# Kernel optimization log

Hardware: AMD Instinct MI355X
Metric: run time of the kernel (lower is better)

Reference implementation:

```python
import jax, jax.numpy as jnp
import numpy as np

HEADS = 16
D_MODEL = 1024
D_K = D_MODEL // HEADS
BATCH = 4
SEQ = 1024
NEG_BIG = -1000000000.0


def setup_inputs() -> dict:
    key = jax.random.key(0)
    ks = jax.random.split(key, 7)
    s = 1.0 / np.sqrt(D_MODEL)
    return {
        "q": jax.random.normal(ks[0], (BATCH, SEQ, D_MODEL), jnp.float32),
        "k": jax.random.normal(ks[1], (BATCH, SEQ, D_MODEL), jnp.float32),
        "v": jax.random.normal(ks[2], (BATCH, SEQ, D_MODEL), jnp.float32),
        "Wq": jax.random.normal(ks[3], (D_MODEL, D_MODEL), jnp.float32) * s,
        "Wk": jax.random.normal(ks[4], (D_MODEL, D_MODEL), jnp.float32) * s,
        "Wv": jax.random.normal(ks[5], (D_MODEL, D_MODEL), jnp.float32) * s,
        "Wo": jax.random.normal(ks[6], (D_MODEL, D_MODEL), jnp.float32) * s,
    }


def reference(q, k, v, Wq, Wk, Wv, Wo):
    bs = q.shape[0]
    residual = q
    # torch Linear(bias=False): x @ W.T ; then the module's quirky reshape
    # view(bs, h, -1, d_k) on the contiguous [bs, seq, d_model] buffer.
    qh = (q @ Wq.T).reshape(bs, HEADS, -1, D_K)   # [b, h, s, d_k]
    kh = (k @ Wk.T).reshape(bs, HEADS, -1, D_K)
    vh = (v @ Wv.T).reshape(bs, HEADS, -1, D_K)
    scores = jnp.einsum("bhqd,bhkd->bhqk", qh, kh) / jnp.sqrt(
        jnp.asarray(D_K, qh.dtype))
    # data-dependent mask: exact-zero scores get -1e9 before softmax
    scores = jnp.where(scores == 0, jnp.asarray(NEG_BIG, scores.dtype), scores)
    attn = jax.nn.softmax(scores, axis=-1)  # dropout is identity in eval mode
    out = jnp.einsum("bhqk,bhkd->bhqd", attn, vh)  # [b, h, s, d_k]
    concat = jnp.swapaxes(out, 1, 2).reshape(bs, -1, D_MODEL)
    return concat @ Wo.T + residual
```

## Files before the change

### kernel.cpp

```cpp
#include <hip/hip_runtime.h>
#include <stdint.h>

typedef __bf16 bf16x8 __attribute__((ext_vector_type(8)));
typedef __bf16 bf16x2v __attribute__((ext_vector_type(2)));
typedef float f32x4 __attribute__((ext_vector_type(4)));
typedef uint16_t u16x8 __attribute__((ext_vector_type(8)));
typedef uint16_t u16x4 __attribute__((ext_vector_type(4)));

#define DMODEL 1024
#define K1SC 0.1803368801111244f

__device__ __forceinline__ uint16_t bfc(float f) {
  __bf16 h = (__bf16)f;
  return __builtin_bit_cast(uint16_t, h);
}
__device__ __forceinline__ uint32_t pk32(float a, float b) {
  bf16x2v t = {(__bf16)a, (__bf16)b};
  return __builtin_bit_cast(uint32_t, t);
}
__device__ __forceinline__ void gld16(const void* src, void* dst) {
  __builtin_amdgcn_global_load_lds((const __attribute__((address_space(1))) void*)src,
                                   (__attribute__((address_space(3))) void*)dst, 16, 0, 0);
}

__global__ void cvt_all_kernel(const float* __restrict__ q, const float* __restrict__ k,
                               const float* __restrict__ v, const float* __restrict__ Wq,
                               const float* __restrict__ Wk, const float* __restrict__ Wv,
                               const float* __restrict__ Wo, uint16_t* __restrict__ qb,
                               uint16_t* __restrict__ kb, uint16_t* __restrict__ vb,
                               uint16_t* __restrict__ Wqb, uint16_t* __restrict__ Wkb,
                               uint16_t* __restrict__ Wvb, uint16_t* __restrict__ Wob) {
  int bid = blockIdx.x;
  const float* src;
  uint16_t* dst;
  int off;
  if (bid < 12288) {
    int s = bid >> 12;
    src = s == 0 ? q : (s == 1 ? k : v);
    dst = s == 0 ? qb : (s == 1 ? kb : vb);
    off = bid & 4095;
  } else {
    int r = bid - 12288;
    int s = r >> 10;
    src = s == 0 ? Wq : (s == 1 ? Wk : (s == 2 ? Wv : Wo));
    dst = s == 0 ? Wqb : (s == 1 ? Wkb : (s == 2 ? Wvb : Wob));
    off = r & 1023;
  }
  int i = off * 256 + threadIdx.x;
  f32x4 x = ((const f32x4*)src)[i];
  u16x4 r;
#pragma unroll
  for (int j = 0; j < 4; ++j) r[j] = bfc(x[j]);
  ((u16x4*)dst)[i] = r;
}

__global__ __launch_bounds__(256, 2)
void gemm_qkv_kernel(const uint16_t* __restrict__ A0, const uint16_t* __restrict__ A1,
                     const uint16_t* __restrict__ A2, const uint16_t* __restrict__ W0,
                     const uint16_t* __restrict__ W1, const uint16_t* __restrict__ W2,
                     uint16_t* __restrict__ C0, uint16_t* __restrict__ C1,
                     uint16_t* __restrict__ C2) {
  const int z = blockIdx.z;
  const uint16_t* A = z == 0 ? A0 : (z == 1 ? A1 : A2);
  const uint16_t* Bw = z == 0 ? W0 : (z == 1 ? W1 : W2);
  uint16_t* C = z == 0 ? C0 : (z == 1 ? C1 : C2);
  const float osc = (z == 0) ? K1SC : 1.0f;
  __shared__ __align__(16) uint16_t As[2][128 * 32];
  __shared__ __align__(16) uint16_t Bs[2][128 * 32];
  const int t = threadIdx.x;
  const int lane = t & 63;
  const int w = t >> 6;
  const int wr = w >> 1, wc = w & 1;
  const int m0 = blockIdx.y * 128, n0 = blockIdx.x * 128;
  const int lr = lane & 15, ksl = lane >> 4;

  f32x4 acc[4][4];
#pragma unroll
  for (int m = 0; m < 4; ++m)
#pragma unroll
    for (int n = 0; n < 4; ++n) acc[m][n] = (f32x4){0.f, 0.f, 0.f, 0.f};

  auto stage = [&](int buf, int k0) {
#pragma unroll
    for (int cc = 0; cc < 2; ++cc) {
      int idx = cc * 256 + t;
      int row = idx >> 2, sl = idx & 3;
      gld16(A + (size_t)(m0 + row) * DMODEL + k0 + sl * 8, &As[buf][idx * 8]);
      gld16(Bw + (size_t)(n0 + row) * DMODEL + k0 + sl * 8, &Bs[buf][idx * 8]);
    }
  };

  stage(0, 0);
  __syncthreads();

  int cur = 0;
#pragma unroll 1
  for (int kt = 0; kt < 32; ++kt) {
    if (kt < 31) stage(cur ^ 1, (kt + 1) * 32);
    bf16x8 af[4], bfv[4];
#pragma unroll
    for (int m = 0; m < 4; ++m)
      af[m] = *(const bf16x8*)&As[cur][(wr * 64 + m * 16 + lr) * 32 + ksl * 8];
#pragma unroll
    for (int n = 0; n < 4; ++n)
      bfv[n] = *(const bf16x8*)&Bs[cur][(wc * 64 + n * 16 + lr) * 32 + ksl * 8];
    __builtin_amdgcn_s_setprio(1);
#pragma unroll
    for (int m = 0; m < 4; ++m)
#pragma unroll
      for (int n = 0; n < 4; ++n)
        acc[m][n] = __builtin_amdgcn_mfma_f32_16x16x32_bf16(af[m], bfv[n], acc[m][n], 0, 0, 0);
    __builtin_amdgcn_s_setprio(0);
    __syncthreads();
    cur ^= 1;
  }

#pragma unroll
  for (int m = 0; m < 4; ++m) {
#pragma unroll
    for (int n = 0; n < 4; ++n) {
      int col = n0 + wc * 64 + n * 16 + lr;
#pragma unroll
      for (int r = 0; r < 4; ++r) {
        int row = m0 + wr * 64 + m * 16 + ksl * 4 + r;
        C[(size_t)row * DMODEL + col] = bfc(acc[m][n][r] * osc);
      }
    }
  }
}

__global__ __launch_bounds__(256, 2)
void gemm_bt_kernel(const uint16_t* __restrict__ A, const uint16_t* __restrict__ Bw,
                    float* __restrict__ Cf, const float* __restrict__ resid) {
  __shared__ __align__(16) uint16_t As[2][64 * 32];
  __shared__ __align__(16) uint16_t Bs[2][128 * 32];
  const int t = threadIdx.x;
  const int lane = t & 63;
  const int w = t >> 6;
  const int wr = w >> 1, wc = w & 1;
  const int m0 = blockIdx.y * 64, n0 = blockIdx.x * 128;
  const int lr = lane & 15, ksl = lane >> 4;

  f32x4 acc[2][4];
#pragma unroll
  for (int m = 0; m < 2; ++m)
#pragma unroll
    for (int n = 0; n < 4; ++n) acc[m][n] = (f32x4){0.f, 0.f, 0.f, 0.f};

  {
    int row = t >> 2, sl = t & 3;
    gld16(A + (size_t)(m0 + row) * DMODEL + sl * 8, &As[0][t * 8]);
#pragma unroll
    for (int cc = 0; cc < 2; ++cc) {
      int c = t + cc * 256;
      int rb = c >> 2, slb = c & 3;
      gld16(Bw + (size_t)(n0 + rb) * DMODEL + slb * 8, &Bs[0][c * 8]);
    }
  }
  __syncthreads();

  int cur = 0;
#pragma unroll 1
  for (int kt = 0; kt < 32; ++kt) {
    if (kt < 31) {
      int k0 = (kt + 1) * 32;
      int nb = cur ^ 1;
      int row = t >> 2, sl = t & 3;
      gld16(A + (size_t)(m0 + row) * DMODEL + k0 + sl * 8, &As[nb][t * 8]);
#pragma unroll
      for (int cc = 0; cc < 2; ++cc) {
        int c = t + cc * 256;
        int rb = c >> 2, slb = c & 3;
        gld16(Bw + (size_t)(n0 + rb) * DMODEL + k0 + slb * 8, &Bs[nb][c * 8]);
      }
    }
    bf16x8 af[2], bfv[4];
#pragma unroll
    for (int m = 0; m < 2; ++m)
      af[m] = *(const bf16x8*)&As[cur][(wr * 32 + m * 16 + lr) * 32 + ksl * 8];
#pragma unroll
    for (int n = 0; n < 4; ++n)
      bfv[n] = *(const bf16x8*)&Bs[cur][(wc * 64 + n * 16 + lr) * 32 + ksl * 8];
    __builtin_amdgcn_s_setprio(1);
#pragma unroll
    for (int m = 0; m < 2; ++m)
#pragma unroll
      for (int n = 0; n < 4; ++n)
        acc[m][n] = __builtin_amdgcn_mfma_f32_16x16x32_bf16(af[m], bfv[n], acc[m][n], 0, 0, 0);
    __builtin_amdgcn_s_setprio(0);
    __syncthreads();
    cur ^= 1;
  }

#pragma unroll
  for (int m = 0; m < 2; ++m) {
#pragma unroll
    for (int n = 0; n < 4; ++n) {
      int col = n0 + wc * 64 + n * 16 + lr;
#pragma unroll
      for (int r = 0; r < 4; ++r) {
        int row = m0 + wr * 32 + m * 16 + ksl * 4 + r;
        size_t idx = (size_t)row * DMODEL + col;
        Cf[idx] = acc[m][n][r] + resid[idx];
      }
    }
  }
}

__global__ __launch_bounds__(256, 2)
void attn_mfma_kernel(const uint16_t* __restrict__ Pq, const uint16_t* __restrict__ Pk,
                      const uint16_t* __restrict__ Pv, uint16_t* __restrict__ Cc) {
  __shared__ __align__(16) uint16_t Ks[2][64 * 64];
  __shared__ __align__(16) uint16_t Vts[2][64 * 64];
  __shared__ __align__(16) uint16_t Ps[4][16 * 64];

  const int t = threadIdx.x;
  const int w = t >> 6;
  const int lane = t & 63;
  const int lr = lane & 15;
  const int ksl = lane >> 4;
  const int qt = blockIdx.x;
  const int bh = blockIdx.y;
  const int b = bh >> 4, h = bh & 15;

  const uint16_t* Qb = Pq + (size_t)bh * 65536 + (size_t)qt * 64 * 64;
  const uint16_t* Kb = Pk + (size_t)bh * 65536;
  const uint16_t* Vb = Pv + (size_t)bh * 65536;

  bf16x8 qf[2];
  {
    const uint16_t* qrow = Qb + (size_t)(w * 16 + lr) * 64 + ksl * 8;
    qf[0] = *(const bf16x8*)(qrow);
    qf[1] = *(const bf16x8*)(qrow + 32);
  }

  f32x4 Oa[4];
#pragma unroll
  for (int n = 0; n < 4; ++n) Oa[n] = (f32x4){0.f, 0.f, 0.f, 0.f};
  f32x4 lsum4 = {0.f, 0.f, 0.f, 0.f};

  const int p2 = t & 31;
  const int c8 = t >> 5;
  const int sw = (lr & 7) << 4;
  u16x8 va, vb2;

  auto stageK = [&](int buf, int kt) {
#pragma unroll
    for (int cc = 0; cc < 2; ++cc) {
      int idx = cc * 256 + t;
      int row = idx >> 3;
      int bo = (idx & 7) * 16;
      int srcb = bo ^ ((row & 7) << 4);
      gld16(Kb + (size_t)(kt * 64 + row) * 64 + (srcb >> 1), &Ks[buf][idx * 8]);
    }
  };
  auto loadV = [&](int kt) {
    const uint16_t* s0 = Vb + (size_t)(kt * 64 + p2 * 2) * 64 + c8 * 8;
    va = *(const u16x8*)s0;
    vb2 = *(const u16x8*)(s0 + 64);
  };
  auto writeV = [&](int buf) {
    char* base = (char*)&Vts[buf][0];
#pragma unroll
    for (int i = 0; i < 8; ++i) {
      int d = c8 * 8 + i;
      uint32_t val = (uint32_t)va[i] | ((uint32_t)vb2[i] << 16);
      *(uint32_t*)(base + d * 128 + ((p2 * 4) ^ ((d & 7) << 4))) = val;
    }
  };

  stageK(0, 0);
  loadV(0);
  writeV(0);
  __syncthreads();

  int cur = 0;
#pragma unroll 1
  for (int kt = 0; kt < 16; ++kt) {
    if (kt < 15) { stageK(cur ^ 1, kt + 1); loadV(kt + 1); }

    f32x4 S[4];
#pragma unroll
    for (int n = 0; n < 4; ++n) S[n] = (f32x4){0.f, 0.f, 0.f, 0.f};
    __builtin_amdgcn_s_setprio(1);
#pragma unroll
    for (int n = 0; n < 4; ++n) {
      const char* kbp = (const char*)&Ks[cur][0] + (n * 16 + lr) * 128;
#pragma unroll
      for (int c = 0; c < 2; ++c) {
        bf16x8 kf = *(const bf16x8*)(kbp + ((c * 64 + ksl * 16) ^ sw));
        S[n] = __builtin_amdgcn_mfma_f32_16x16x32_bf16(kf, qf[c], S[n], 0, 0, 0);
      }
    }
    __builtin_amdgcn_s_setprio(0);

    f32x4 psum = {0.f, 0.f, 0.f, 0.f};
    f32x4 p4[4];
#pragma unroll
    for (int n = 0; n < 4; ++n) {
#pragma unroll
      for (int r = 0; r < 4; ++r) {
        float x = S[n][r];
        float e = __builtin_amdgcn_exp2f(x);
        p4[n][r] = (x == 0.f) ? 0.f : e;
      }
      psum += p4[n];
    }
    lsum4 += psum;

    char* pb = (char*)&Ps[w][0] + lr * 128;
#pragma unroll
    for (int n = 0; n < 4; ++n) {
      int co = (n * 16 + ksl * 4) * 2;
      *(uint32_t*)(pb + (co ^ sw)) = pk32(p4[n][0], p4[n][1]);
      *(uint32_t*)(pb + ((co + 4) ^ sw)) = pk32(p4[n][2], p4[n][3]);
    }

    __builtin_amdgcn_s_setprio(1);
#pragma unroll
    for (int c = 0; c < 2; ++c) {
      bf16x8 pf = *(const bf16x8*)(pb + ((c * 64 + ksl * 16) ^ sw));
#pragma unroll
      for (int n = 0; n < 4; ++n) {
        const char* vbp = (const char*)&Vts[cur][0] + (n * 16 + lr) * 128;
        bf16x8 vf = *(const bf16x8*)(vbp + ((c * 64 + ksl * 16) ^ sw));
        Oa[n] = __builtin_amdgcn_mfma_f32_16x16x32_bf16(pf, vf, Oa[n], 0, 0, 0);
      }
    }
    __builtin_amdgcn_s_setprio(0);

    if (kt < 15) writeV(cur ^ 1);
    __syncthreads();
    cur ^= 1;
  }

  float lrow = (lsum4[0] + lsum4[1]) + (lsum4[2] + lsum4[3]);
  lrow += __shfl_xor(lrow, 16);
  lrow += __shfl_xor(lrow, 32);
  f32x4 inv4;
#pragma unroll
  for (int r = 0; r < 4; ++r) inv4[r] = 1.f / __shfl(lrow, ksl * 4 + r);

  uint16_t* dst = Cc + (size_t)b * 1048576 + (size_t)(qt * 64 + w * 16) * 1024 + h * 64;
#pragma unroll
  for (int r = 0; r < 4; ++r) {
    int qq = ksl * 4 + r;
#pragma unroll
    for (int n = 0; n < 4; ++n) {
      dst[qq * 1024 + n * 16 + lr] = bfc(Oa[n][r] * inv4[r]);
    }
  }
}

extern "C" void kernel_launch(void* const* d_in, const int* in_sizes, int n_in,
                              void* d_out, int out_size, void* d_ws, size_t ws_size,
                              hipStream_t stream) {
  const float* q  = (const float*)d_in[0];
  const float* k  = (const float*)d_in[1];
  const float* v  = (const float*)d_in[2];
  const float* Wq = (const float*)d_in[3];
  const float* Wk = (const float*)d_in[4];
  const float* Wv = (const float*)d_in[5];
  const float* Wo = (const float*)d_in[6];
  float* out = (float*)d_out;
  char* ws = (char*)d_ws;
  const size_t MB = 1u << 20;
  uint16_t* qb  = (uint16_t*)(ws + 0 * MB);
  uint16_t* kb  = (uint16_t*)(ws + 8 * MB);
  uint16_t* vb  = (uint16_t*)(ws + 16 * MB);
  uint16_t* Wqb = (uint16_t*)(ws + 24 * MB);
  uint16_t* Wkb = (uint16_t*)(ws + 26 * MB);
  uint16_t* Wvb = (uint16_t*)(ws + 28 * MB);
  uint16_t* Wob = (uint16_t*)(ws + 30 * MB);
  uint16_t* Pq  = (uint16_t*)(ws + 32 * MB);
  uint16_t* Pk  = (uint16_t*)(ws + 40 * MB);
  uint16_t* Pv  = (uint16_t*)(ws + 48 * MB);
  uint16_t* Cc  = (uint16_t*)(ws + 56 * MB);

  cvt_all_kernel<<<16384, 256, 0, stream>>>(q, k, v, Wq, Wk, Wv, Wo,
                                            qb, kb, vb, Wqb, Wkb, Wvb, Wob);

  gemm_qkv_kernel<<<dim3(8, 32, 3), 256, 0, stream>>>(qb, kb, vb, Wqb, Wkb, Wvb,
                                                      Pq, Pk, Pv);

  attn_mfma_kernel<<<dim3(16, 64), 256, 0, stream>>>(Pq, Pk, Pv, Cc);

  gemm_bt_kernel<<<dim3(8, 64), 256, 0, stream>>>(Cc, Wob, out, q);
}
```

Measured before the change: 116.9 us.

## Deepen GEMM K-tiles to 64 with XOR-swizzled LDS and XCD-aware block remapping

Both projection GEMMs now stage 64-wide K tiles, which halves the number of main-loop iterations and barriers. Each 16-byte chunk's K offset is XOR-swizzled by row so the LDS fragment reads avoid bank conflicts. Blocks are launched on a 1D grid and remapped so that consecutive tiles land on the same XCD, for better L2 reuse. The output GEMM also grows from 64x128 to 128x128 tiles, which doubles LDS use per block and halves the grid to 256 blocks, risking lower occupancy and fewer waves in flight.

```diff
diff --git a/kernel.cpp b/kernel.cpp
--- a/kernel.cpp
+++ b/kernel.cpp
@@ -60,19 +60,25 @@
                      const uint16_t* __restrict__ W1, const uint16_t* __restrict__ W2,
                      uint16_t* __restrict__ C0, uint16_t* __restrict__ C1,
                      uint16_t* __restrict__ C2) {
-  const int z = blockIdx.z;
+  int orig = blockIdx.x;
+  int lin = (orig & 7) * 96 + (orig >> 3);
+  int z = lin >> 8;
+  int rem = lin & 255;
+  int m0 = (rem >> 3) * 128, n0 = (rem & 7) * 128;
+
   const uint16_t* A = z == 0 ? A0 : (z == 1 ? A1 : A2);
   const uint16_t* Bw = z == 0 ? W0 : (z == 1 ? W1 : W2);
   uint16_t* C = z == 0 ? C0 : (z == 1 ? C1 : C2);
   const float osc = (z == 0) ? K1SC : 1.0f;
-  __shared__ __align__(16) uint16_t As[2][128 * 32];
-  __shared__ __align__(16) uint16_t Bs[2][128 * 32];
+
+  __shared__ __align__(16) uint16_t As[2][128 * 64];
+  __shared__ __align__(16) uint16_t Bs[2][128 * 64];
   const int t = threadIdx.x;
   const int lane = t & 63;
   const int w = t >> 6;
   const int wr = w >> 1, wc = w & 1;
-  const int m0 = blockIdx.y * 128, n0 = blockIdx.x * 128;
   const int lr = lane & 15, ksl = lane >> 4;
+  const int sw = (lr & 7) << 4;
 
   f32x4 acc[4][4];
 #pragma unroll
@@ -82,11 +88,18 @@
 
   auto stage = [&](int buf, int k0) {
 #pragma unroll
-    for (int cc = 0; cc < 2; ++cc) {
+    for (int cc = 0; cc < 4; ++cc) {
       int idx = cc * 256 + t;
-      int row = idx >> 2, sl = idx & 3;
-      gld16(A + (size_t)(m0 + row) * DMODEL + k0 + sl * 8, &As[buf][idx * 8]);
-      gld16(Bw + (size_t)(n0 + row) * DMODEL + k0 + sl * 8, &Bs[buf][idx * 8]);
+      int row = idx >> 3, ch = idx & 7;
+      int so = ((ch * 16) ^ ((row & 7) << 4)) >> 1;
+      gld16(A + (size_t)(m0 + row) * DMODEL + k0 + so, &As[buf][idx * 8]);
+    }
+#pragma unroll
+    for (int cc = 0; cc < 4; ++cc) {
+      int idx = cc * 256 + t;
+      int row = idx >> 3, ch = idx & 7;
+      int so = ((ch * 16) ^ ((row & 7) << 4)) >> 1;
+      gld16(Bw + (size_t)(n0 + row) * DMODEL + k0 + so, &Bs[buf][idx * 8]);
     }
   };
 
@@ -95,21 +108,29 @@
 
   int cur = 0;
 #pragma unroll 1
-  for (int kt = 0; kt < 32; ++kt) {
-    if (kt < 31) stage(cur ^ 1, (kt + 1) * 32);
-    bf16x8 af[4], bfv[4];
-#pragma unroll
-    for (int m = 0; m < 4; ++m)
-      af[m] = *(const bf16x8*)&As[cur][(wr * 64 + m * 16 + lr) * 32 + ksl * 8];
-#pragma unroll
-    for (int n = 0; n < 4; ++n)
-      bfv[n] = *(const bf16x8*)&Bs[cur][(wc * 64 + n * 16 + lr) * 32 + ksl * 8];
+  for (int kt = 0; kt < 16; ++kt) {
+    if (kt < 15) stage(cur ^ 1, (kt + 1) * 64);
+    const char* Ab = (const char*)&As[cur][0];
+    const char* Bb = (const char*)&Bs[cur][0];
+    bf16x8 af[2][4], bfv[2][4];
+#pragma unroll
+    for (int c = 0; c < 2; ++c) {
+      int co = ((c * 4 + ksl) * 16) ^ sw;
+#pragma unroll
+      for (int m = 0; m < 4; ++m)
+        af[c][m] = *(const bf16x8*)(Ab + (wr * 64 + m * 16 + lr) * 128 + co);
+#pragma unroll
+      for (int n = 0; n < 4; ++n)
+        bfv[c][n] = *(const bf16x8*)(Bb + (wc * 64 + n * 16 + lr) * 128 + co);
+    }
     __builtin_amdgcn_s_setprio(1);
 #pragma unroll
-    for (int m = 0; m < 4; ++m)
-#pragma unroll
-      for (int n = 0; n < 4; ++n)
-        acc[m][n] = __builtin_amdgcn_mfma_f32_16x16x32_bf16(af[m], bfv[n], acc[m][n], 0, 0, 0);
+    for (int c = 0; c < 2; ++c)
+#pragma unroll
+      for (int m = 0; m < 4; ++m)
+#pragma unroll
+        for (int n = 0; n < 4; ++n)
+          acc[m][n] = __builtin_amdgcn_mfma_f32_16x16x32_bf16(af[c][m], bfv[c][n], acc[m][n], 0, 0, 0);
     __builtin_amdgcn_s_setprio(0);
     __syncthreads();
     cur ^= 1;
@@ -130,76 +151,85 @@
 }
 
 __global__ __launch_bounds__(256, 2)
-void gemm_bt_kernel(const uint16_t* __restrict__ A, const uint16_t* __restrict__ Bw,
-                    float* __restrict__ Cf, const float* __restrict__ resid) {
-  __shared__ __align__(16) uint16_t As[2][64 * 32];
-  __shared__ __align__(16) uint16_t Bs[2][128 * 32];
+void gemm_o_kernel(const uint16_t* __restrict__ A, const uint16_t* __restrict__ Bw,
+                   float* __restrict__ Cf, const float* __restrict__ resid) {
+  int orig = blockIdx.x;
+  int lin = (orig & 7) * 32 + (orig >> 3);
+  int m0 = (lin >> 3) * 128, n0 = (lin & 7) * 128;
+
+  __shared__ __align__(16) uint16_t As[2][128 * 64];
+  __shared__ __align__(16) uint16_t Bs[2][128 * 64];
   const int t = threadIdx.x;
   const int lane = t & 63;
   const int w = t >> 6;
   const int wr = w >> 1, wc = w & 1;
-  const int m0 = blockIdx.y * 64, n0 = blockIdx.x * 128;
   const int lr = lane & 15, ksl = lane >> 4;
-
-  f32x4 acc[2][4];
-#pragma unroll
-  for (int m = 0; m < 2; ++m)
+  const int sw = (lr & 7) << 4;
+
+  f32x4 acc[4][4];
+#pragma unroll
+  for (int m = 0; m < 4; ++m)
 #pragma unroll
     for (int n = 0; n < 4; ++n) acc[m][n] = (f32x4){0.f, 0.f, 0.f, 0.f};
 
-  {
-    int row = t >> 2, sl = t & 3;
-    gld16(A + (size_t)(m0 + row) * DMODEL + sl * 8, &As[0][t * 8]);
-#pragma unroll
-    for (int cc = 0; cc < 2; ++cc) {
-      int c = t + cc * 256;
-      int rb = c >> 2, slb = c & 3;
-      gld16(Bw + (size_t)(n0 + rb) * DMODEL + slb * 8, &Bs[0][c * 8]);
-    }
-  }
+  auto stage = [&](int buf, int k0) {
+#pragma unroll
+    for (int cc = 0; cc < 4; ++cc) {
+      int idx = cc * 256 + t;
+      int row = idx >> 3, ch = idx & 7;
+      int so = ((ch * 16) ^ ((row & 7) << 4)) >> 1;
+      gld16(A + (size_t)(m0 + row) * DMODEL + k0 + so, &As[buf][idx * 8]);
+    }
+#pragma unroll
+    for (int cc = 0; cc < 4; ++cc) {
+      int idx = cc * 256 + t;
+      int row = idx >> 3, ch = idx & 7;
+      int so = ((ch * 16) ^ ((row & 7) << 4)) >> 1;
+      gld16(Bw + (size_t)(n0 + row) * DMODEL + k0 + so, &Bs[buf][idx * 8]);
+    }
+  };
+
+  stage(0, 0);
   __syncthreads();
 
   int cur = 0;
 #pragma unroll 1
-  for (int kt = 0; kt < 32; ++kt) {
-    if (kt < 31) {
-      int k0 = (kt + 1) * 32;
-      int nb = cur ^ 1;
-      int row = t >> 2, sl = t & 3;
-      gld16(A + (size_t)(m0 + row) * DMODEL + k0 + sl * 8, &As[nb][t * 8]);
-#pragma unroll
-      for (int cc = 0; cc < 2; ++cc) {
-        int c = t + cc * 256;
-        int rb = c >> 2, slb = c & 3;
-        gld16(Bw + (size_t)(n0 + rb) * DMODEL + k0 + slb * 8, &Bs[nb][c * 8]);
-      }
-    }
-    bf16x8 af[2], bfv[4];
-#pragma unroll
-    for (int m = 0; m < 2; ++m)
-      af[m] = *(const bf16x8*)&As[cur][(wr * 32 + m * 16 + lr) * 32 + ksl * 8];
-#pragma unroll
-    for (int n = 0; n < 4; ++n)
-      bfv[n] = *(const bf16x8*)&Bs[cur][(wc * 64 + n * 16 + lr) * 32 + ksl * 8];
+  for (int kt = 0; kt < 16; ++kt) {
+    if (kt < 15) stage(cur ^ 1, (kt + 1) * 64);
+    const char* Ab = (const char*)&As[cur][0];
+    const char* Bb = (const char*)&Bs[cur][0];
+    bf16x8 af[2][4], bfv[2][4];
+#pragma unroll
+    for (int c = 0; c < 2; ++c) {
+      int co = ((c * 4 + ksl) * 16) ^ sw;
+#pragma unroll
+      for (int m = 0; m < 4; ++m)
+        af[c][m] = *(const bf16x8*)(Ab + (wr * 64 + m * 16 + lr) * 128 + co);
+#pragma unroll
+      for (int n = 0; n < 4; ++n)
+        bfv[c][n] = *(const bf16x8*)(Bb + (wc * 64 + n * 16 + lr) * 128 + co);
+    }
     __builtin_amdgcn_s_setprio(1);
 #pragma unroll
-    for (int m = 0; m < 2; ++m)
-#pragma unroll
-      for (int n = 0; n < 4; ++n)
-        acc[m][n] = __builtin_amdgcn_mfma_f32_16x16x32_bf16(af[m], bfv[n], acc[m][n], 0, 0, 0);
+    for (int c = 0; c < 2; ++c)
+#pragma unroll
+      for (int m = 0; m < 4; ++m)
+#pragma unroll
+        for (int n = 0; n < 4; ++n)
+          acc[m][n] = __builtin_amdgcn_mfma_f32_16x16x32_bf16(af[c][m], bfv[c][n], acc[m][n], 0, 0, 0);
     __builtin_amdgcn_s_setprio(0);
     __syncthreads();
     cur ^= 1;
   }
 
 #pragma unroll
-  for (int m = 0; m < 2; ++m) {
+  for (int m = 0; m < 4; ++m) {
 #pragma unroll
     for (int n = 0; n < 4; ++n) {
       int col = n0 + wc * 64 + n * 16 + lr;
 #pragma unroll
       for (int r = 0; r < 4; ++r) {
-        int row = m0 + wr * 32 + m * 16 + ksl * 4 + r;
+        int row = m0 + wr * 64 + m * 16 + ksl * 4 + r;
         size_t idx = (size_t)row * DMODEL + col;
         Cf[idx] = acc[m][n][r] + resid[idx];
       }
@@ -380,10 +410,10 @@
   cvt_all_kernel<<<16384, 256, 0, stream>>>(q, k, v, Wq, Wk, Wv, Wo,
                                             qb, kb, vb, Wqb, Wkb, Wvb, Wob);
 
-  gemm_qkv_kernel<<<dim3(8, 32, 3), 256, 0, stream>>>(qb, kb, vb, Wqb, Wkb, Wvb,
-                                                      Pq, Pk, Pv);
+  gemm_qkv_kernel<<<768, 256, 0, stream>>>(qb, kb, vb, Wqb, Wkb, Wvb,
+                                           Pq, Pk, Pv);
 
   attn_mfma_kernel<<<dim3(16, 64), 256, 0, stream>>>(Pq, Pk, Pv, Cc);
 
-  gemm_bt_kernel<<<dim3(8, 64), 256, 0, stream>>>(Cc, Wob, out, q);
-}
+  gemm_o_kernel<<<256, 256, 0, stream>>>(Cc, Wob, out, q);
+}
```

Result: faster. 112.8 us (-3.5%).

## Swizzle GEMM LDS layout and remap block IDs for XCD locality

Applied to the files above, without the earlier changes.

Applies an XOR swizzle to the 16-byte chunks staged into LDS by both GEMM kernels, so the per-lane fragment reads avoid bank conflicts. All three main kernels now launch on a 1D grid and remap block IDs so consecutive logical tiles land on the same XCD (stride-8 round robin), which is meant to improve L2 reuse of shared A/B rows and K/V tiles. Swizzle correctness depends on the load-side and read-side XOR patterns matching, and the remap assumes an 8-XCD dispatch order.

```diff
diff --git a/kernel.cpp b/kernel.cpp
--- a/kernel.cpp
+++ b/kernel.cpp
@@ -60,19 +60,25 @@
                      const uint16_t* __restrict__ W1, const uint16_t* __restrict__ W2,
                      uint16_t* __restrict__ C0, uint16_t* __restrict__ C1,
                      uint16_t* __restrict__ C2) {
-  const int z = blockIdx.z;
+  int orig = blockIdx.x;
+  int lin = (orig & 7) * 96 + (orig >> 3);
+  int z = lin >> 8;
+  int rem = lin & 255;
+  int m0 = (rem >> 3) * 128, n0 = (rem & 7) * 128;
+
   const uint16_t* A = z == 0 ? A0 : (z == 1 ? A1 : A2);
   const uint16_t* Bw = z == 0 ? W0 : (z == 1 ? W1 : W2);
   uint16_t* C = z == 0 ? C0 : (z == 1 ? C1 : C2);
   const float osc = (z == 0) ? K1SC : 1.0f;
+
   __shared__ __align__(16) uint16_t As[2][128 * 32];
   __shared__ __align__(16) uint16_t Bs[2][128 * 32];
   const int t = threadIdx.x;
   const int lane = t & 63;
   const int w = t >> 6;
   const int wr = w >> 1, wc = w & 1;
-  const int m0 = blockIdx.y * 128, n0 = blockIdx.x * 128;
   const int lr = lane & 15, ksl = lane >> 4;
+  const int sw2 = (lr & 3) << 4;
 
   f32x4 acc[4][4];
 #pragma unroll
@@ -84,9 +90,16 @@
 #pragma unroll
     for (int cc = 0; cc < 2; ++cc) {
       int idx = cc * 256 + t;
-      int row = idx >> 2, sl = idx & 3;
-      gld16(A + (size_t)(m0 + row) * DMODEL + k0 + sl * 8, &As[buf][idx * 8]);
-      gld16(Bw + (size_t)(n0 + row) * DMODEL + k0 + sl * 8, &Bs[buf][idx * 8]);
+      int row = idx >> 2, ch = idx & 3;
+      int so = ((ch * 16) ^ ((row & 3) << 4)) >> 1;
+      gld16(A + (size_t)(m0 + row) * DMODEL + k0 + so, &As[buf][idx * 8]);
+    }
+#pragma unroll
+    for (int cc = 0; cc < 2; ++cc) {
+      int idx = cc * 256 + t;
+      int row = idx >> 2, ch = idx & 3;
+      int so = ((ch * 16) ^ ((row & 3) << 4)) >> 1;
+      gld16(Bw + (size_t)(n0 + row) * DMODEL + k0 + so, &Bs[buf][idx * 8]);
     }
   };
 
@@ -97,13 +110,16 @@
 #pragma unroll 1
   for (int kt = 0; kt < 32; ++kt) {
     if (kt < 31) stage(cur ^ 1, (kt + 1) * 32);
+    const char* Ab = (const char*)&As[cur][0];
+    const char* Bb = (const char*)&Bs[cur][0];
+    const int co = (ksl * 16) ^ sw2;
     bf16x8 af[4], bfv[4];
 #pragma unroll
     for (int m = 0; m < 4; ++m)
-      af[m] = *(const bf16x8*)&As[cur][(wr * 64 + m * 16 + lr) * 32 + ksl * 8];
+      af[m] = *(const bf16x8*)(Ab + (wr * 64 + m * 16 + lr) * 64 + co);
 #pragma unroll
     for (int n = 0; n < 4; ++n)
-      bfv[n] = *(const bf16x8*)&Bs[cur][(wc * 64 + n * 16 + lr) * 32 + ksl * 8];
+      bfv[n] = *(const bf16x8*)(Bb + (wc * 64 + n * 16 + lr) * 64 + co);
     __builtin_amdgcn_s_setprio(1);
 #pragma unroll
     for (int m = 0; m < 4; ++m)
@@ -130,16 +146,20 @@
 }
 
 __global__ __launch_bounds__(256, 2)
-void gemm_bt_kernel(const uint16_t* __restrict__ A, const uint16_t* __restrict__ Bw,
-                    float* __restrict__ Cf, const float* __restrict__ resid) {
+void gemm_o_kernel(const uint16_t* __restrict__ A, const uint16_t* __restrict__ Bw,
+                   float* __restrict__ Cf, const float* __restrict__ resid) {
+  int orig = blockIdx.x;
+  int lin = (orig & 7) * 64 + (orig >> 3);
+  int m0 = (lin >> 3) * 64, n0 = (lin & 7) * 128;
+
   __shared__ __align__(16) uint16_t As[2][64 * 32];
   __shared__ __align__(16) uint16_t Bs[2][128 * 32];
   const int t = threadIdx.x;
   const int lane = t & 63;
   const int w = t >> 6;
   const int wr = w >> 1, wc = w & 1;
-  const int m0 = blockIdx.y * 64, n0 = blockIdx.x * 128;
   const int lr = lane & 15, ksl = lane >> 4;
+  const int sw2 = (lr & 3) << 4;
 
   f32x4 acc[2][4];
 #pragma unroll
@@ -147,40 +167,38 @@
 #pragma unroll
     for (int n = 0; n < 4; ++n) acc[m][n] = (f32x4){0.f, 0.f, 0.f, 0.f};
 
-  {
-    int row = t >> 2, sl = t & 3;
-    gld16(A + (size_t)(m0 + row) * DMODEL + sl * 8, &As[0][t * 8]);
+  auto stage = [&](int buf, int k0) {
+    {
+      int row = t >> 2, ch = t & 3;
+      int so = ((ch * 16) ^ ((row & 3) << 4)) >> 1;
+      gld16(A + (size_t)(m0 + row) * DMODEL + k0 + so, &As[buf][t * 8]);
+    }
 #pragma unroll
     for (int cc = 0; cc < 2; ++cc) {
-      int c = t + cc * 256;
-      int rb = c >> 2, slb = c & 3;
-      gld16(Bw + (size_t)(n0 + rb) * DMODEL + slb * 8, &Bs[0][c * 8]);
-    }
-  }
+      int idx = cc * 256 + t;
+      int row = idx >> 2, ch = idx & 3;
+      int so = ((ch * 16) ^ ((row & 3) << 4)) >> 1;
+      gld16(Bw + (size_t)(n0 + row) * DMODEL + k0 + so, &Bs[buf][idx * 8]);
+    }
+  };
+
+  stage(0, 0);
   __syncthreads();
 
   int cur = 0;
 #pragma unroll 1
   for (int kt = 0; kt < 32; ++kt) {
-    if (kt < 31) {
-      int k0 = (kt + 1) * 32;
-      int nb = cur ^ 1;
-      int row = t >> 2, sl = t & 3;
-      gld16(A + (size_t)(m0 + row) * DMODEL + k0 + sl * 8, &As[nb][t * 8]);
-#pragma unroll
-      for (int cc = 0; cc < 2; ++cc) {
-        int c = t + cc * 256;
-        int rb = c >> 2, slb = c & 3;
-        gld16(Bw + (size_t)(n0 + rb) * DMODEL + k0 + slb * 8, &Bs[nb][c * 8]);
-      }
-    }
+    if (kt < 31) stage(cur ^ 1, (kt + 1) * 32);
+    const char* Ab = (const char*)&As[cur][0];
+    const char* Bb = (const char*)&Bs[cur][0];
+    const int co = (ksl * 16) ^ sw2;
     bf16x8 af[2], bfv[4];
 #pragma unroll
     for (int m = 0; m < 2; ++m)
-      af[m] = *(const bf16x8*)&As[cur][(wr * 32 + m * 16 + lr) * 32 + ksl * 8];
+      af[m] = *(const bf16x8*)(Ab + (wr * 32 + m * 16 + lr) * 64 + co);
 #pragma unroll
     for (int n = 0; n < 4; ++n)
-      bfv[n] = *(const bf16x8*)&Bs[cur][(wc * 64 + n * 16 + lr) * 32 + ksl * 8];
+      bfv[n] = *(const bf16x8*)(Bb + (wc * 64 + n * 16 + lr) * 64 + co);
     __builtin_amdgcn_s_setprio(1);
 #pragma unroll
     for (int m = 0; m < 2; ++m)
@@ -219,8 +237,9 @@
   const int lane = t & 63;
   const int lr = lane & 15;
   const int ksl = lane >> 4;
-  const int qt = blockIdx.x;
-  const int bh = blockIdx.y;
+  int orig = blockIdx.x;
+  int lin = (orig & 7) * 128 + (orig >> 3);
+  const int bh = lin >> 4, qt = lin & 15;
   const int b = bh >> 4, h = bh & 15;
 
   const uint16_t* Qb = Pq + (size_t)bh * 65536 + (size_t)qt * 64 * 64;
@@ -380,10 +399,10 @@
   cvt_all_kernel<<<16384, 256, 0, stream>>>(q, k, v, Wq, Wk, Wv, Wo,
                                             qb, kb, vb, Wqb, Wkb, Wvb, Wob);
 
-  gemm_qkv_kernel<<<dim3(8, 32, 3), 256, 0, stream>>>(qb, kb, vb, Wqb, Wkb, Wvb,
-                                                      Pq, Pk, Pv);
-
-  attn_mfma_kernel<<<dim3(16, 64), 256, 0, stream>>>(Pq, Pk, Pv, Cc);
-
-  gemm_bt_kernel<<<dim3(8, 64), 256, 0, stream>>>(Cc, Wob, out, q);
-}
+  gemm_qkv_kernel<<<768, 256, 0, stream>>>(qb, kb, vb, Wqb, Wkb, Wvb,
+                                           Pq, Pk, Pv);
+
+  attn_mfma_kernel<<<1024, 256, 0, stream>>>(Pq, Pk, Pv, Cc);
+
+  gemm_o_kernel<<<512, 256, 0, stream>>>(Cc, Wob, out, q);
+}
```

Measured after the change: 107.1 us. 8.3% less time.
